# Optimization experiments

Measured on AMD Instinct MI355X. Metric: run time of the kernel, lower is better.

Reference implementation:

```python
import math
import jax, jax.numpy as jnp
import numpy as np

B, T, D = 2, 2048, 1024
NH = 16
HD = D // NH


def setup_inputs() -> dict:
    key = jax.random.key(0)
    k1, k2, k3 = jax.random.split(key, 3)
    s = 0.02
    return {
        "x": jax.random.normal(k1, (B, T, D), dtype=jnp.float32),
        "w_qkv": jax.random.normal(k2, (D, 3 * D), dtype=jnp.float32) * s,
        "w_proj": jax.random.normal(k3, (D, D), dtype=jnp.float32) * s,
    }


def reference(x, w_qkv, w_proj):
    b, t, c = x.shape
    qkv = x @ w_qkv  # [B,T,3D]
    q, k, v = jnp.split(qkv, 3, axis=-1)
    # [B,NH,T,HD]
    q = q.reshape(b, t, NH, HD).transpose(0, 2, 1, 3)
    k = k.reshape(b, t, NH, HD).transpose(0, 2, 1, 3)
    v = v.reshape(b, t, NH, HD).transpose(0, 2, 1, 3)
    scores = jnp.einsum("bhqd,bhkd->bhqk", q, k) / math.sqrt(HD)
    mask = jnp.tril(jnp.ones((t, t), dtype=x.dtype))  # [T,T]
    # faithful to source: scaled scores are multiplied by the mask, then -1e9 added where masked
    masked = scores * mask + (1.0 - mask) * (-1e9)
    a = jax.nn.softmax(masked, axis=-1)
    out = jnp.einsum("bhqk,bhkd->bhqd", a, v)  # [B,NH,T,HD]
    out = out.transpose(0, 2, 1, 3).reshape(b, t, c)
    return out @ w_proj
```

## Files before the change

kernel.cpp:

```cpp
#include <hip/hip_runtime.h>
#include <stdint.h>

#define B_SZ 2
#define T_SEQ 2048
#define D_MODEL 1024
#define NHEADS 16
#define HDIM 64
#define QKV_P (3 * D_MODEL)

typedef unsigned short u16;
typedef uint32_t u32;
typedef __attribute__((ext_vector_type(4))) float f32x4;
typedef __attribute__((ext_vector_type(8))) short s16x8;
typedef __attribute__((ext_vector_type(4))) short s16x4;

__device__ __forceinline__ u16 f2bf(float f) {
  union { float f; uint32_t u; } v; v.f = f;
  uint32_t r = v.u + 0x7fffu + ((v.u >> 16) & 1u);
  return (u16)(r >> 16);
}

__device__ __forceinline__ float fastexp2(float x) {
  float r;
  asm volatile("v_exp_f32 %0, %1" : "=v"(r) : "v"(x));
  return r;
}

__device__ __forceinline__ u32 cvtpk(float lo, float hi) {
  u32 r;
  asm volatile("v_cvt_pk_bf16_f32 %0, %1, %2" : "=v"(r) : "v"(lo), "v"(hi));
  return r;
}

__device__ __forceinline__ void async16(const void* g, void* l) {
  __builtin_amdgcn_global_load_lds((const __attribute__((address_space(1))) void*)g,
                                   (__attribute__((address_space(3))) void*)l,
                                   16, 0, 0);
}

__device__ __forceinline__ void rawbar() {
  __builtin_amdgcn_s_barrier();
  __builtin_amdgcn_sched_barrier(0);
}

__global__ __launch_bounds__(256) void prep(const float* __restrict__ x,
                                            const float* __restrict__ wq,
                                            const float* __restrict__ wp,
                                            u16* __restrict__ xb,
                                            u16* __restrict__ wqkvT,
                                            u16* __restrict__ wprojT) {
  const int bid = blockIdx.x, tid = threadIdx.x;
  if (bid < 4096) {
    int i = bid * 256 + tid;
    float4 v = ((const float4*)x)[i];
    ushort4 o;
    o.x = f2bf(v.x); o.y = f2bf(v.y); o.z = f2bf(v.z); o.w = f2bf(v.w);
    ((ushort4*)xb)[i] = o;
    return;
  }
  __shared__ float tile[32][33];
  const float* in; u16* outp; int C, bx, by;
  if (bid < 4096 + 3072) {
    int bb = bid - 4096; in = wq; outp = wqkvT; C = 3072; bx = bb % 96; by = bb / 96;
  } else {
    int bb = bid - 7168; in = wp; outp = wprojT; C = 1024; bx = bb % 32; by = bb / 32;
  }
  const int tx = tid & 31, ty = tid >> 5;
  const int c0 = bx * 32, r0 = by * 32;
#pragma unroll
  for (int i = 0; i < 4; i++)
    tile[ty + i * 8][tx] = in[(size_t)(r0 + ty + i * 8) * C + c0 + tx];
  __syncthreads();
#pragma unroll
  for (int i = 0; i < 4; i++)
    outp[(size_t)(c0 + ty + i * 8) * D_MODEL + r0 + tx] = f2bf(tile[tx][ty + i * 8]);
}

template <int F32OUT, int VFUSE, int NBN>
__global__ __launch_bounds__(256, 2) void gemm128(const u16* __restrict__ A,
                                                  const u16* __restrict__ BT,
                                                  void* __restrict__ Cout,
                                                  u16* __restrict__ vTout,
                                                  int N) {
  __shared__ u16 As[2][128 * 64];
  __shared__ u16 Bs[2][128 * 64];
  const int tid = threadIdx.x;
  const int lane = tid & 63, w = tid >> 6;
  const int l15 = lane & 15, g = lane >> 4;
  const int wr = w >> 1, wc = w & 1;
  const int id = blockIdx.x;
  const int cid = id >> 3;
  const int bm = (id & 7) * 4 + cid / NBN;
  const int bn = cid % NBN;
  const int K = 1024;
  const u16* Ab = A + (size_t)bm * 128 * K;
  const u16* Bb = BT + (size_t)bn * 128 * K;
  f32x4 acc[4][4];
#pragma unroll
  for (int i = 0; i < 4; i++)
#pragma unroll
    for (int j = 0; j < 4; j++) acc[i][j] = (f32x4){0.f, 0.f, 0.f, 0.f};

#define G1_LD(dst, srcb, kt_)                                                \
  do {                                                                       \
    _Pragma("unroll") for (int i_ = 0; i_ < 4; i_++) {                       \
      int o_ = (tid + i_ * 256) * 16;                                        \
      int lo_ = o_ ^ (((o_ >> 7) & 7) << 4);                                 \
      async16((srcb) + (size_t)(lo_ >> 7) * K + (kt_) + ((lo_ & 127) >> 1),  \
              (char*)(dst) + o_);                                            \
    }                                                                        \
  } while (0)

  G1_LD(As[0], Ab, 0);
  G1_LD(Bs[0], Bb, 0);
  int cur = 0;
  for (int t = 0; t < 16; t++) {
    if (t < 15) {
      G1_LD(As[cur ^ 1], Ab, (t + 1) * 64);
      G1_LD(Bs[cur ^ 1], Bb, (t + 1) * 64);
      asm volatile("s_waitcnt vmcnt(8)" ::: "memory");
    } else {
      asm volatile("s_waitcnt vmcnt(0)" ::: "memory");
    }
    rawbar();
    s16x8 af[4][2], bf[4][2];
#pragma unroll
    for (int i = 0; i < 4; i++) {
      int r_ = wr * 64 + i * 16 + l15;
#pragma unroll
      for (int kk = 0; kk < 2; kk++)
        af[i][kk] = *(const s16x8*)((const char*)As[cur] +
                                    ((r_ * 128 + kk * 64 + g * 16) ^ ((r_ & 7) << 4)));
    }
#pragma unroll
    for (int jn = 0; jn < 4; jn++) {
      int n_ = wc * 64 + jn * 16 + l15;
#pragma unroll
      for (int kk = 0; kk < 2; kk++)
        bf[jn][kk] = *(const s16x8*)((const char*)Bs[cur] +
                                     ((n_ * 128 + kk * 64 + g * 16) ^ ((n_ & 7) << 4)));
    }
    __builtin_amdgcn_s_setprio(1);
#pragma unroll
    for (int i = 0; i < 4; i++)
#pragma unroll
      for (int jn = 0; jn < 4; jn++) {
        acc[i][jn] = __builtin_amdgcn_mfma_f32_16x16x32_bf16(af[i][0], bf[jn][0], acc[i][jn], 0, 0, 0);
        acc[i][jn] = __builtin_amdgcn_mfma_f32_16x16x32_bf16(af[i][1], bf[jn][1], acc[i][jn], 0, 0, 0);
      }
    __builtin_amdgcn_s_setprio(0);
    rawbar();
    cur ^= 1;
  }

  if (VFUSE && bn >= 16) {
#pragma unroll
    for (int i = 0; i < 4; i++) {
      const int m = bm * 128 + wr * 64 + i * 16 + g * 4;
      const int bloc = m >> 11;
      const int tl = m & 2047;
#pragma unroll
      for (int jn = 0; jn < 4; jn++) {
        const int hh = bn * 128 + wc * 64 + jn * 16 + l15 - 2048;
        uint2 pk;
        pk.x = cvtpk(acc[i][jn][0], acc[i][jn][1]);
        pk.y = cvtpk(acc[i][jn][2], acc[i][jn][3]);
        *(uint2*)&vTout[(size_t)(bloc * 1024 + hh) * T_SEQ + tl] = pk;
      }
    }
    return;
  }
#pragma unroll
  for (int i = 0; i < 4; i++) {
    const int row0 = bm * 128 + wr * 64 + i * 16 + g * 4;
#pragma unroll
    for (int jn = 0; jn < 4; jn++) {
      const int col = bn * 128 + wc * 64 + jn * 16 + l15;
#pragma unroll
      for (int r = 0; r < 4; r++) {
        if (F32OUT)
          ((float*)Cout)[(size_t)(row0 + r) * N + col] = acc[i][jn][r];
        else
          ((u16*)Cout)[(size_t)(row0 + r) * N + col] = f2bf(acc[i][jn][r]);
      }
    }
  }
}

__global__ __launch_bounds__(256, 4) void flash_attn(const u16* __restrict__ qkv,
                                                     const u16* __restrict__ vT,
                                                     u16* __restrict__ attn) {
  __shared__ u16 Ks[2][64 * 64];
  __shared__ u16 Vs[2][64 * 64];
  const int tid = threadIdx.x;
  const int lane = tid & 63, w = tid >> 6;
  const int l15 = lane & 15, g = lane >> 4;
  const int id = blockIdx.x;
  const int bh = ((id & 7) << 2) | ((id >> 3) & 3);
  const int j = (id >> 5) & 7, k4 = (id >> 8) & 3;
  const int qs = (k4 == 0) ? (31 - j) : (k4 == 1) ? (16 + j) : (k4 == 2) ? (15 - j) : j;
  const int b = bh >> 4, h = bh & 15;

  const size_t qrow = (size_t)(b * T_SEQ + qs * 64 + w * 16 + l15);
  s16x8 qf[2];
  qf[0] = *(const s16x8*)(qkv + qrow * QKV_P + h * HDIM + 0 * 32 + g * 8);
  qf[1] = *(const s16x8*)(qkv + qrow * QKV_P + h * HDIM + 1 * 32 + g * 8);

  f32x4 O[4];
#pragma unroll
  for (int t = 0; t < 4; t++) O[t] = (f32x4){0.f, 0.f, 0.f, 0.f};
  f32x4 sumacc = (f32x4){0.f, 0.f, 0.f, 0.f};
  float m_s = -1e30f;
  const int qrl = w * 16 + l15;
  const float sc = 0.18033688011112042f;
  const s16x4 onesf = {(short)0x3F80, (short)0x3F80, (short)0x3F80, (short)0x3F80};

#define STAGE(buf, kvt_)                                                                     \
  do {                                                                                       \
    _Pragma("unroll") for (int i_ = 0; i_ < 2; i_++) {                                       \
      int o_ = (tid + i_ * 256) * 16;                                                        \
      int lo_ = o_ ^ (((o_ >> 7) & 7) << 4);                                                 \
      int row_ = lo_ >> 7;                                                                   \
      int byt_ = lo_ & 127;                                                                  \
      async16(qkv + (size_t)(b * T_SEQ + (kvt_) * 64 + row_) * QKV_P + D_MODEL + h * HDIM +  \
                  (byt_ >> 1),                                                               \
              (char*)Ks[buf] + o_);                                                          \
      async16(vT + (size_t)(bh * HDIM + row_) * T_SEQ + (kvt_) * 64 + (byt_ >> 1),           \
              (char*)Vs[buf] + o_);                                                          \
    }                                                                                        \
  } while (0)

  STAGE(0, 0);
  int cur = 0;
  const int nt = qs + 1;
  for (int kvt = 0; kvt < nt; ++kvt) {
    if (kvt < qs) {
      STAGE(cur ^ 1, kvt + 1);
      asm volatile("s_waitcnt vmcnt(4)" ::: "memory");
    } else {
      asm volatile("s_waitcnt vmcnt(0)" ::: "memory");
    }
    rawbar();

    f32x4 S[4];
#pragma unroll
    for (int t16 = 0; t16 < 4; t16++) S[t16] = (f32x4){0.f, 0.f, 0.f, 0.f};
#pragma unroll
    for (int t16 = 0; t16 < 4; t16++)
#pragma unroll
      for (int kk = 0; kk < 2; kk++) {
        int key = t16 * 16 + l15;
        int bp = (key * 128 + kk * 64 + g * 16) ^ ((key & 7) << 4);
        s16x8 kf = *(const s16x8*)((const char*)Ks[cur] + bp);
        S[t16] = __builtin_amdgcn_mfma_f32_16x16x32_bf16(kf, qf[kk], S[t16], 0, 0, 0);
      }

    if (kvt == qs) {
#pragma unroll
      for (int t16 = 0; t16 < 4; t16++)
#pragma unroll
        for (int r = 0; r < 4; r++)
          if (t16 * 16 + g * 4 + r > qrl) S[t16][r] = -3e38f;
    }
    float pmx = fmaxf(fmaxf(fmaxf(S[0][0], S[0][1]), fmaxf(S[0][2], S[0][3])),
                      fmaxf(fmaxf(S[1][0], S[1][1]), fmaxf(S[1][2], S[1][3])));
    pmx = fmaxf(pmx, fmaxf(fmaxf(fmaxf(S[2][0], S[2][1]), fmaxf(S[2][2], S[2][3])),
                           fmaxf(fmaxf(S[3][0], S[3][1]), fmaxf(S[3][2], S[3][3]))));
    if (!__all(pmx - m_s <= 40.f)) {
      float mx = fmaxf(pmx, __shfl_xor(pmx, 16));
      mx = fmaxf(mx, __shfl_xor(mx, 32));
      const float mnew = fmaxf(m_s, mx);
      const float alpha = fastexp2((m_s - mnew) * sc);
      m_s = mnew;
      sumacc[0] *= alpha; sumacc[1] *= alpha; sumacc[2] *= alpha; sumacc[3] *= alpha;
#pragma unroll
      for (int t = 0; t < 4; t++)
#pragma unroll
        for (int r = 0; r < 4; r++) O[t][r] *= alpha;
    }
    const float msc = m_s * sc;
    float p[16];
#pragma unroll
    for (int t16 = 0; t16 < 4; t16++)
#pragma unroll
      for (int r = 0; r < 4; r++) p[t16 * 4 + r] = fastexp2(fmaf(S[t16][r], sc, -msc));

#pragma unroll
    for (int t16 = 0; t16 < 4; t16++) {
      union { u32 u[2]; s16x4 v; } pbv;
      pbv.u[0] = cvtpk(p[t16 * 4 + 0], p[t16 * 4 + 1]);
      pbv.u[1] = cvtpk(p[t16 * 4 + 2], p[t16 * 4 + 3]);
      sumacc = __builtin_amdgcn_mfma_f32_16x16x16bf16_1k(onesf, pbv.v, sumacc, 0, 0, 0);
#pragma unroll
      for (int t = 0; t < 4; t++) {
        int hd = t * 16 + l15;
        int bp = (hd * 128 + t16 * 32 + g * 8) ^ ((hd & 7) << 4);
        s16x4 vf = *(const s16x4*)((const char*)Vs[cur] + bp);
        O[t] = __builtin_amdgcn_mfma_f32_16x16x16bf16_1k(vf, pbv.v, O[t], 0, 0, 0);
      }
    }
    rawbar();
    cur ^= 1;
  }

  const float inv = 1.0f / sumacc[0];
  const size_t row = (size_t)(b * T_SEQ + qs * 64 + w * 16 + l15);
#pragma unroll
  for (int t = 0; t < 4; t++)
#pragma unroll
    for (int pr = 0; pr < 2; pr++) {
      u32 pk = cvtpk(O[t][pr * 2 + 0] * inv, O[t][pr * 2 + 1] * inv);
      *(u32*)&attn[row * D_MODEL + h * HDIM + t * 16 + g * 4 + pr * 2] = pk;
    }
}

extern "C" void kernel_launch(void* const* d_in, const int* in_sizes, int n_in,
                              void* d_out, int out_size, void* d_ws, size_t ws_size,
                              hipStream_t stream) {
  const float* x = (const float*)d_in[0];
  const float* w_qkv = (const float*)d_in[1];
  const float* w_proj = (const float*)d_in[2];
  float* out = (float*)d_out;
  char* ws = (char*)d_ws;
  const size_t MB = (size_t)1 << 20;
  if (ws_size < 56 * MB) return;
  u16* xb = (u16*)(ws + 0);
  u16* wqkvT = (u16*)(ws + 8 * MB);
  u16* wprojT = (u16*)(ws + 14 * MB);
  u16* qkv = (u16*)(ws + 16 * MB);
  u16* vT = (u16*)(ws + 40 * MB);
  u16* attn = (u16*)(ws + 48 * MB);

  prep<<<8192, 256, 0, stream>>>(x, w_qkv, w_proj, xb, wqkvT, wprojT);
  gemm128<0, 1, 24><<<768, 256, 0, stream>>>(xb, wqkvT, qkv, vT, QKV_P);
  flash_attn<<<1024, 256, 0, stream>>>(qkv, vT, attn);
  gemm128<1, 0, 8><<<256, 256, 0, stream>>>(attn, wprojT, out, nullptr, D_MODEL);
}
```

Measured before the change: 108.3 us.

## Interleave next-tile async loads with per-row MFMA phases in QKV GEMM

Splits the GEMM main loop into four phases, one per A row-block, with a barrier after each. The next K-tile's global-to-LDS copies are issued in halves between phases instead of all at the start, which spreads memory traffic across the MFMA work. A fragments are now loaded per phase rather than all up front, which lowers register pressure. The cost is three extra barriers per K-step and a tighter vmcnt wait that may expose load latency.

```diff
diff --git a/kernel.cpp b/kernel.cpp
--- a/kernel.cpp
+++ b/kernel.cpp
@@ -101,55 +101,65 @@
 #pragma unroll
     for (int j = 0; j < 4; j++) acc[i][j] = (f32x4){0.f, 0.f, 0.f, 0.f};
 
-#define G1_LD(dst, srcb, kt_)                                                \
-  do {                                                                       \
-    _Pragma("unroll") for (int i_ = 0; i_ < 4; i_++) {                       \
-      int o_ = (tid + i_ * 256) * 16;                                        \
-      int lo_ = o_ ^ (((o_ >> 7) & 7) << 4);                                 \
-      async16((srcb) + (size_t)(lo_ >> 7) * K + (kt_) + ((lo_ & 127) >> 1),  \
-              (char*)(dst) + o_);                                            \
-    }                                                                        \
+#define LDH(dstbase, srcb, h_, kt_)                                           \
+  do {                                                                        \
+    _Pragma("unroll") for (int i_ = 0; i_ < 2; i_++) {                        \
+      int o_ = (h_)*8192 + (tid + i_ * 256) * 16;                             \
+      int lo_ = o_ ^ (((o_ >> 7) & 7) << 4);                                  \
+      async16((srcb) + (size_t)(lo_ >> 7) * K + (kt_) + ((lo_ & 127) >> 1),   \
+              (char*)(dstbase) + o_);                                         \
+    }                                                                         \
   } while (0)
 
-  G1_LD(As[0], Ab, 0);
-  G1_LD(Bs[0], Bb, 0);
+#define PHASE(i_)                                                             \
+  {                                                                           \
+    int r_ = wr * 64 + (i_)*16 + l15;                                         \
+    s16x8 a0 = *(const s16x8*)((const char*)As[cur] +                         \
+                               ((r_ * 128 + g * 16) ^ ((r_ & 7) << 4)));      \
+    s16x8 a1 = *(const s16x8*)((const char*)As[cur] +                         \
+                               ((r_ * 128 + 64 + g * 16) ^ ((r_ & 7) << 4))); \
+    __builtin_amdgcn_s_setprio(1);                                            \
+    _Pragma("unroll") for (int jn = 0; jn < 4; jn++) {                        \
+      acc[i_][jn] =                                                           \
+          __builtin_amdgcn_mfma_f32_16x16x32_bf16(a0, bf[jn][0], acc[i_][jn], 0, 0, 0); \
+      acc[i_][jn] =                                                           \
+          __builtin_amdgcn_mfma_f32_16x16x32_bf16(a1, bf[jn][1], acc[i_][jn], 0, 0, 0); \
+    }                                                                         \
+    __builtin_amdgcn_s_setprio(0);                                            \
+    rawbar();                                                                 \
+  }
+
+  LDH(As[0], Ab, 0, 0);
+  LDH(As[0], Ab, 1, 0);
+  LDH(Bs[0], Bb, 0, 0);
+  LDH(Bs[0], Bb, 1, 0);
   int cur = 0;
   for (int t = 0; t < 16; t++) {
-    if (t < 15) {
-      G1_LD(As[cur ^ 1], Ab, (t + 1) * 64);
-      G1_LD(Bs[cur ^ 1], Bb, (t + 1) * 64);
-      asm volatile("s_waitcnt vmcnt(8)" ::: "memory");
+    const bool pf = (t < 15);
+    const int ktn = (t + 1) * 64;
+    if (pf) {
+      LDH(Bs[cur ^ 1], Bb, 0, ktn);
+      asm volatile("s_waitcnt vmcnt(2)" ::: "memory");
     } else {
       asm volatile("s_waitcnt vmcnt(0)" ::: "memory");
     }
     rawbar();
-    s16x8 af[4][2], bf[4][2];
-#pragma unroll
-    for (int i = 0; i < 4; i++) {
-      int r_ = wr * 64 + i * 16 + l15;
-#pragma unroll
-      for (int kk = 0; kk < 2; kk++)
-        af[i][kk] = *(const s16x8*)((const char*)As[cur] +
-                                    ((r_ * 128 + kk * 64 + g * 16) ^ ((r_ & 7) << 4)));
-    }
+    s16x8 bf[4][2];
 #pragma unroll
     for (int jn = 0; jn < 4; jn++) {
       int n_ = wc * 64 + jn * 16 + l15;
-#pragma unroll
-      for (int kk = 0; kk < 2; kk++)
-        bf[jn][kk] = *(const s16x8*)((const char*)Bs[cur] +
-                                     ((n_ * 128 + kk * 64 + g * 16) ^ ((n_ & 7) << 4)));
-    }
-    __builtin_amdgcn_s_setprio(1);
-#pragma unroll
-    for (int i = 0; i < 4; i++)
-#pragma unroll
-      for (int jn = 0; jn < 4; jn++) {
-        acc[i][jn] = __builtin_amdgcn_mfma_f32_16x16x32_bf16(af[i][0], bf[jn][0], acc[i][jn], 0, 0, 0);
-        acc[i][jn] = __builtin_amdgcn_mfma_f32_16x16x32_bf16(af[i][1], bf[jn][1], acc[i][jn], 0, 0, 0);
-      }
-    __builtin_amdgcn_s_setprio(0);
-    rawbar();
+      bf[jn][0] = *(const s16x8*)((const char*)Bs[cur] +
+                                  ((n_ * 128 + g * 16) ^ ((n_ & 7) << 4)));
+      bf[jn][1] = *(const s16x8*)((const char*)Bs[cur] +
+                                  ((n_ * 128 + 64 + g * 16) ^ ((n_ & 7) << 4)));
+    }
+    PHASE(0);
+    if (pf) LDH(Bs[cur ^ 1], Bb, 1, ktn);
+    PHASE(1);
+    if (pf) LDH(As[cur ^ 1], Ab, 0, ktn);
+    PHASE(2);
+    if (pf) LDH(As[cur ^ 1], Ab, 1, ktn);
+    PHASE(3);
     cur ^= 1;
   }
 
```

Result: slower. 136.0 us (+25.6%).
